# Performance work log

Hardware: AMD Instinct MI355X
Metric: run time of the kernel (lower is better)

## Reference

```python
import jax, jax.numpy as jnp
import numpy as np

NEG = -9e15

def _gat_layer(x, adj, W, a_src, a_dst):
    # x: [B,N,Fin], W: [Fin,Fout], a_src/a_dst: [Fout], adj: [N,N]
    h = jnp.einsum('bnf,fo->bno', x, W)                    # [B,N,Fout]
    e_src = jnp.einsum('bno,o->bn', h, a_src)              # [B,N]
    e_dst = jnp.einsum('bno,o->bn', h, a_dst)              # [B,N]
    e = jax.nn.leaky_relu(e_src[:, :, None] + e_dst[:, None, :], 0.2)  # [B,N,N]
    att = jax.nn.softmax(jnp.where(adj > 0, e, NEG), axis=-1)
    return jnp.einsum('bij,bjo->bio', att, h)              # [B,N,Fout]

def setup_inputs() -> dict:
    key = jax.random.key(0)
    ks = jax.random.split(key, 12)
    B, N, Fin = 8, 2048, 128
    H = [128, 128, 64]
    C = 128
    s = lambda *d: 1.0 / np.sqrt(d[0])
    inp = {
        'x':   jax.random.normal(ks[0], (B, N, Fin), jnp.float32),
        'adj': jax.random.normal(ks[1], (N, N), jnp.float32),
        'W1':  jax.random.normal(ks[2], (Fin, H[0]), jnp.float32) * s(Fin),
        'a1s': jax.random.normal(ks[3], (H[0],), jnp.float32) * s(H[0]),
        'a1d': jax.random.normal(ks[4], (H[0],), jnp.float32) * s(H[0]),
        'W2':  jax.random.normal(ks[5], (H[0], H[1]), jnp.float32) * s(H[0]),
        'a2s': jax.random.normal(ks[6], (H[1],), jnp.float32) * s(H[1]),
        'a2d': jax.random.normal(ks[7], (H[1],), jnp.float32) * s(H[1]),
        'W3':  jax.random.normal(ks[8], (H[1], H[2]), jnp.float32) * s(H[1]),
        'a3s': jax.random.normal(ks[9], (H[2],), jnp.float32) * s(H[2]),
        'a3d': jax.random.normal(ks[10], (H[2],), jnp.float32) * s(H[2]),
        'Wlin': jax.random.normal(ks[11], (H[2] * N, C), jnp.float32) * s(H[2] * N),
        'blin': jnp.zeros((C,), jnp.float32),
    }
    return inp

def reference(x, adj, W1, a1s, a1d, W2, a2s, a2d, W3, a3s, a3d, Wlin, blin):
    out = jax.nn.relu(_gat_layer(x, adj, W1, a1s, a1d))
    out = jax.nn.relu(_gat_layer(out, adj, W2, a2s, a2d))
    out = jax.nn.relu(_gat_layer(out, adj, W3, a3s, a3d))
    B = out.shape[0]
    out = out.reshape(B, -1)              # flatten [B, N*H3]
    return out @ Wlin + blin              # [B, num_classes]
```

## Files before the change

kernel.cpp:

```cpp
#include <hip/hip_runtime.h>
#include <stdint.h>


typedef unsigned short u16;
typedef __bf16 bf16x8 __attribute__((ext_vector_type(8)));
typedef float f32x4 __attribute__((ext_vector_type(4)));
typedef u16 u16x8 __attribute__((ext_vector_type(8)));

#define LOG2E 1.44269504088896340736f

__device__ __forceinline__ float b2f(u16 u) {
    union { unsigned int i; float f; } v; v.i = ((unsigned int)u) << 16; return v.f;
}
__device__ __forceinline__ u16 f2b(float f) {
    union { float f; unsigned int i; } v; v.f = f;
    unsigned int i = v.i;
    return (u16)((i + 0x7fffu + ((i >> 16) & 1u)) >> 16);
}
__device__ __forceinline__ float fast_exp2(float x) {
#if __has_builtin(__builtin_amdgcn_exp2f)
    return __builtin_amdgcn_exp2f(x);
#else
    return exp2f(x);
#endif
}

union ABfrag { bf16x8 v; u16x8 u; };

__device__ __forceinline__ void gload_lds16(const u16* g, u16* l) {
    __builtin_amdgcn_global_load_lds((const __attribute__((address_space(1))) void*)g,
                                     (__attribute__((address_space(3))) void*)l,
                                     16, 0, 0);
}

__global__ void __launch_bounds__(256) k_mask(const float* __restrict__ adj,
                                              uint32_t* __restrict__ adjm) {
    const int w = threadIdx.x >> 6, lane = threadIdx.x & 63;
    const int row = blockIdx.x * 4 + w;
    const float* ar = adj + (size_t)row * 2048;
    uint32_t* mr = adjm + (size_t)row * 64;
    for (int j0 = 0; j0 < 2048; j0 += 64) {
        unsigned long long m = __ballot(ar[j0 + lane] > 0.f);
        if (lane == 0) {
            mr[(j0 >> 5)] = (uint32_t)m;
            mr[(j0 >> 5) + 1] = (uint32_t)(m >> 32);
        }
    }
}

__global__ void k_prep(const float* __restrict__ W1, const float* __restrict__ W2,
                       const float* __restrict__ W3,
                       const float* __restrict__ a1s, const float* __restrict__ a1d,
                       const float* __restrict__ a2s, const float* __restrict__ a2d,
                       const float* __restrict__ a3s, const float* __restrict__ a3d,
                       u16* __restrict__ Wt1, u16* __restrict__ Wt2, u16* __restrict__ Wt3,
                       float* __restrict__ u1s, float* __restrict__ u1d,
                       float* __restrict__ u2s, float* __restrict__ u2d,
                       float* __restrict__ u3s, float* __restrict__ u3d) {
    if (blockIdx.x == 160) {
        int f = threadIdx.x;
        if (f < 128) {
            float s1 = 0.f, d1 = 0.f, s2 = 0.f, d2 = 0.f, s3 = 0.f, d3 = 0.f;
            for (int o = 0; o < 128; ++o) { float w = W1[f * 128 + o]; s1 += w * a1s[o]; d1 += w * a1d[o]; }
            for (int o = 0; o < 128; ++o) { float w = W2[f * 128 + o]; s2 += w * a2s[o]; d2 += w * a2d[o]; }
            for (int o = 0; o <  64; ++o) { float w = W3[f *  64 + o]; s3 += w * a3s[o]; d3 += w * a3d[o]; }
            u1s[f] = s1 * LOG2E; u1d[f] = d1 * LOG2E;
            u2s[f] = s2 * LOG2E; u2d[f] = d2 * LOG2E;
            u3s[f] = s3 * LOG2E; u3d[f] = d3 * LOG2E;
        }
        return;
    }
    int idx = blockIdx.x * 256 + threadIdx.x;
    if (idx < 16384) {
        int f = idx >> 7, o = idx & 127;
        Wt1[o * 128 + f] = f2b(W1[idx]);
    } else if (idx < 32768) {
        int j = idx - 16384; int f = j >> 7, o = j & 127;
        Wt2[o * 128 + f] = f2b(W2[j]);
    } else if (idx < 40960) {
        int j = idx - 32768; int f = j >> 6, o = j & 63;
        Wt3[o * 128 + f] = f2b(W3[j]);
    }
}

template <int F, bool XF32>
__global__ void __launch_bounds__(256) k_h(const void* __restrict__ xv,
                                           const u16* __restrict__ Wt,
                                           const float* __restrict__ us,
                                           const float* __restrict__ ud,
                                           u16* __restrict__ h_t,
                                           float* __restrict__ es2,
                                           float* __restrict__ ed2) {
    constexpr int NT = F / 16;
    constexpr int TNP = 72;
    __shared__ __align__(16) u16 hl[F * TNP];

    const int b = blockIdx.x;
    const int nblk = blockIdx.y;
    const int tid = threadIdx.x;
    const int w = tid >> 6, lane = tid & 63;
    const int quad = lane >> 4, l15 = lane & 15;
    const int n0w = nblk * 64 + w * 16;
    const int i_a = n0w + l15;

    ABfrag afr[4];
    float ps = 0.f, pd = 0.f;
    if (XF32) {
        const float* xr = (const float*)xv + ((size_t)(b * 2048 + i_a)) * 128;
#pragma unroll
        for (int kk = 0; kk < 4; ++kk) {
            const int o8 = kk * 32 + quad * 8;
            float4 x0 = *reinterpret_cast<const float4*>(xr + o8);
            float4 x1 = *reinterpret_cast<const float4*>(xr + o8 + 4);
            float4 s0 = *reinterpret_cast<const float4*>(us + o8);
            float4 s1 = *reinterpret_cast<const float4*>(us + o8 + 4);
            float4 d0 = *reinterpret_cast<const float4*>(ud + o8);
            float4 d1 = *reinterpret_cast<const float4*>(ud + o8 + 4);
            ps += x0.x * s0.x + x0.y * s0.y + x0.z * s0.z + x0.w * s0.w
                + x1.x * s1.x + x1.y * s1.y + x1.z * s1.z + x1.w * s1.w;
            pd += x0.x * d0.x + x0.y * d0.y + x0.z * d0.z + x0.w * d0.w
                + x1.x * d1.x + x1.y * d1.y + x1.z * d1.z + x1.w * d1.w;
            afr[kk].u[0] = f2b(x0.x); afr[kk].u[1] = f2b(x0.y);
            afr[kk].u[2] = f2b(x0.z); afr[kk].u[3] = f2b(x0.w);
            afr[kk].u[4] = f2b(x1.x); afr[kk].u[5] = f2b(x1.y);
            afr[kk].u[6] = f2b(x1.z); afr[kk].u[7] = f2b(x1.w);
        }
    } else {
        const u16* xr = (const u16*)xv + ((size_t)(b * 2048 + i_a)) * 128;
#pragma unroll
        for (int kk = 0; kk < 4; ++kk) {
            const int o8 = kk * 32 + quad * 8;
            u16x8 xa = *reinterpret_cast<const u16x8*>(xr + o8);
            afr[kk].u = xa;
            float4 s0 = *reinterpret_cast<const float4*>(us + o8);
            float4 s1 = *reinterpret_cast<const float4*>(us + o8 + 4);
            float4 d0 = *reinterpret_cast<const float4*>(ud + o8);
            float4 d1 = *reinterpret_cast<const float4*>(ud + o8 + 4);
            float xf[8];
#pragma unroll
            for (int j = 0; j < 8; ++j) xf[j] = b2f(xa[j]);
            ps += xf[0] * s0.x + xf[1] * s0.y + xf[2] * s0.z + xf[3] * s0.w
                + xf[4] * s1.x + xf[5] * s1.y + xf[6] * s1.z + xf[7] * s1.w;
            pd += xf[0] * d0.x + xf[1] * d0.y + xf[2] * d0.z + xf[3] * d0.w
                + xf[4] * d1.x + xf[5] * d1.y + xf[6] * d1.z + xf[7] * d1.w;
        }
    }
    ps += __shfl_xor(ps, 16, 64); ps += __shfl_xor(ps, 32, 64);
    pd += __shfl_xor(pd, 16, 64); pd += __shfl_xor(pd, 32, 64);
    if (quad == 0) {
        es2[b * 2048 + i_a] = ps;
        ed2[b * 2048 + i_a] = pd;
    }

    f32x4 acc[NT];
#pragma unroll
    for (int nt = 0; nt < NT; ++nt) acc[nt] = (f32x4){0.f, 0.f, 0.f, 0.f};
#pragma unroll
    for (int kk = 0; kk < 4; ++kk) {
#pragma unroll
        for (int nt = 0; nt < NT; ++nt) {
            bf16x8 bfv = *reinterpret_cast<const bf16x8*>(
                Wt + (nt * 16 + l15) * 128 + kk * 32 + quad * 8);
            acc[nt] = __builtin_amdgcn_mfma_f32_16x16x32_bf16(afr[kk].v, bfv, acc[nt], 0, 0, 0);
        }
    }

#pragma unroll
    for (int nt = 0; nt < NT; ++nt)
#pragma unroll
        for (int r = 0; r < 4; ++r)
            hl[(nt * 16 + l15) * TNP + w * 16 + quad * 4 + r] = f2b(acc[nt][r]);
    __syncthreads();
    if (tid < F * 2) {
        int o = tid >> 1, half = tid & 1;
        const u16* src = hl + o * TNP + half * 32;
        u16* dst = h_t + ((size_t)(b * F + o)) * 2048 + nblk * 64 + half * 32;
#pragma unroll
        for (int c = 0; c < 4; ++c)
            *reinterpret_cast<u16x8*>(dst + c * 8) =
                *reinterpret_cast<const u16x8*>(src + c * 8);
    }
}

template <int F, bool OUT_F32>
__global__ void __launch_bounds__(512) k_attn(const float* __restrict__ es2,
                                              const float* __restrict__ ed2,
                                              const uint32_t* __restrict__ adjm,
                                              const u16* __restrict__ h_t,
                                              void* __restrict__ outp) {
    constexpr int NT = F / 16;
    __shared__ __align__(16) u16 Ht[2][2][F * 64];
    __shared__ float dLDS[2][64];
    float* accLDS = (float*)&Ht[0][0][0];

    const int b = blockIdx.x;
    const int iblk = blockIdx.y;
    const int tid = threadIdx.x;
    const int grp = tid >> 8;
    const int t8 = tid & 255;
    const int w = t8 >> 6;
    const int lane = tid & 63;
    const int quad = lane >> 4, l15 = lane & 15;
    const int i_a = iblk * 64 + w * 16 + l15;

    const float esv = es2[b * 2048 + i_a];
    const float* edb = ed2 + b * 2048;
    const uint2* mrow = (const uint2*)(adjm + (size_t)i_a * 64);
    const u16* hb = h_t + (size_t)b * F * 2048;

    const int lro = lane >> 3;
    const int lcp = lane & 7;
    const int jt0 = grp * 16;

    f32x4 acc[NT];
#pragma unroll
    for (int nt = 0; nt < NT; ++nt) acc[nt] = (f32x4){0.f, 0.f, 0.f, 0.f};
    float dacc = 0.f;

    {
        const int j0 = jt0 * 64;
#pragma unroll
        for (int it = 0; it < F / 32; ++it) {
            int ro = (it * 4 + w) * 8 + lro;
            int c = lcp ^ (ro & 7);
            gload_lds16(hb + (size_t)ro * 2048 + j0 + c * 8, &Ht[grp][0][(it * 4 + w) * 512]);
        }
    }
    float4 ec0 = *reinterpret_cast<const float4*>(edb + jt0 * 64 + quad * 8);
    float4 ec1 = *reinterpret_cast<const float4*>(edb + jt0 * 64 + quad * 8 + 4);
    float4 ec2 = *reinterpret_cast<const float4*>(edb + jt0 * 64 + quad * 8 + 32);
    float4 ec3 = *reinterpret_cast<const float4*>(edb + jt0 * 64 + quad * 8 + 36);
    uint2 mc = mrow[jt0];
    __syncthreads();

    for (int jj = 0; jj < 16; ++jj) {
        const int cur = jj & 1, nxt = cur ^ 1;
        float4 en0, en1, en2, en3; uint2 mn;
        if (jj < 15) {
            const int j1 = (jt0 + jj + 1) * 64;
#pragma unroll
            for (int it = 0; it < F / 32; ++it) {
                int ro = (it * 4 + w) * 8 + lro;
                int c = lcp ^ (ro & 7);
                gload_lds16(hb + (size_t)ro * 2048 + j1 + c * 8, &Ht[grp][nxt][(it * 4 + w) * 512]);
            }
            en0 = *reinterpret_cast<const float4*>(edb + j1 + quad * 8);
            en1 = *reinterpret_cast<const float4*>(edb + j1 + quad * 8 + 4);
            en2 = *reinterpret_cast<const float4*>(edb + j1 + quad * 8 + 32);
            en3 = *reinterpret_cast<const float4*>(edb + j1 + quad * 8 + 36);
            mn = mrow[jt0 + jj + 1];
        }

        ABfrag af[2];
        {
            float ed[16] = {ec0.x, ec0.y, ec0.z, ec0.w, ec1.x, ec1.y, ec1.z, ec1.w,
                            ec2.x, ec2.y, ec2.z, ec2.w, ec3.x, ec3.y, ec3.z, ec3.w};
#pragma unroll
            for (int kk = 0; kk < 2; ++kk) {
                uint32_t word = kk ? mc.y : mc.x;
#pragma unroll
                for (int jx = 0; jx < 8; ++jx) {
                    float e = esv + ed[kk * 8 + jx];
                    float v = fmaxf(e, 0.2f * e);
                    float wv = fast_exp2(v);
                    bool bit = (word >> (quad * 8 + jx)) & 1u;
                    wv = bit ? wv : 0.f;
                    u16 wb = f2b(wv);
                    af[kk].u[jx] = wb;
                    dacc += b2f(wb);
                }
            }
        }

#pragma unroll
        for (int kk = 0; kk < 2; ++kk) {
#pragma unroll
            for (int nt = 0; nt < NT; ++nt) {
                int ob = nt * 16 + l15;
                int c = kk * 4 + quad;
                bf16x8 bfv = *reinterpret_cast<const bf16x8*>(
                    &Ht[grp][cur][ob * 64 + ((c ^ (ob & 7)) * 8)]);
                acc[nt] = __builtin_amdgcn_mfma_f32_16x16x32_bf16(af[kk].v, bfv, acc[nt], 0, 0, 0);
            }
        }

        if (jj < 15) { ec0 = en0; ec1 = en1; ec2 = en2; ec3 = en3; mc = mn; }
        __syncthreads();
    }

    dacc += __shfl_xor(dacc, 16, 64);
    dacc += __shfl_xor(dacc, 32, 64);
    if (quad == 0) dLDS[grp][w * 16 + l15] = dacc;
    if (grp == 1) {
#pragma unroll
        for (int nt = 0; nt < NT; ++nt)
            *reinterpret_cast<f32x4*>(&accLDS[(t8 * NT + nt) * 4]) = acc[nt];
    }
    __syncthreads();
    if (grp == 0) {
#pragma unroll
        for (int nt = 0; nt < NT; ++nt)
            acc[nt] += *reinterpret_cast<const f32x4*>(&accLDS[(t8 * NT + nt) * 4]);
        float dinv[4];
#pragma unroll
        for (int r = 0; r < 4; ++r) {
            int row = w * 16 + quad * 4 + r;
            dinv[r] = 1.0f / fmaxf(dLDS[0][row] + dLDS[1][row], 1e-30f);
        }
        const int ib = iblk * 64 + w * 16 + quad * 4;
        if (OUT_F32) {
            float* o3 = (float*)outp;
#pragma unroll
            for (int nt = 0; nt < NT; ++nt)
#pragma unroll
                for (int r = 0; r < 4; ++r) {
                    float vv = fmaxf(acc[nt][r] * dinv[r], 0.f);
                    o3[((size_t)(b * 2048 + ib + r)) * F + nt * 16 + l15] = vv;
                }
        } else {
            u16* xo = (u16*)outp;
#pragma unroll
            for (int nt = 0; nt < NT; ++nt)
#pragma unroll
                for (int r = 0; r < 4; ++r) {
                    float vv = fmaxf(acc[nt][r] * dinv[r], 0.f);
                    xo[((size_t)(b * 2048 + ib + r)) * F + nt * 16 + l15] = f2b(vv);
                }
        }
    }
}

__global__ void __launch_bounds__(256) k_lin(const float* __restrict__ o3,
                                             const float* __restrict__ Wlin,
                                             float* __restrict__ pbuf) {
    __shared__ float xc[8][256];
    __shared__ float red[8][8][128];
    const int tid = threadIdx.x;
    const int k0 = blockIdx.x * 256;
    for (int idx = tid; idx < 2048; idx += 256) {
        int bb = idx >> 8, kk = idx & 255;
        xc[bb][kk] = o3[(size_t)bb * 131072 + k0 + kk];
    }
    __syncthreads();
    const int o4 = tid & 31;
    const int kb = tid >> 5;
    f32x4 acc[8];
#pragma unroll
    for (int bb = 0; bb < 8; ++bb) acc[bb] = (f32x4){0.f, 0.f, 0.f, 0.f};
    const float* wp = Wlin + (size_t)(k0 + kb * 32) * 128 + o4 * 4;
#pragma unroll 4
    for (int k = 0; k < 32; ++k) {
        f32x4 wv = *reinterpret_cast<const f32x4*>(wp + (size_t)k * 128);
#pragma unroll
        for (int bb = 0; bb < 8; ++bb) acc[bb] += wv * xc[bb][kb * 32 + k];
    }
#pragma unroll
    for (int bb = 0; bb < 8; ++bb)
        *reinterpret_cast<f32x4*>(&red[kb][bb][o4 * 4]) = acc[bb];
    __syncthreads();
    const int f = tid * 4;
    const int bb = f >> 7, o = f & 127;
    f32x4 s = (f32x4){0.f, 0.f, 0.f, 0.f};
#pragma unroll
    for (int k2 = 0; k2 < 8; ++k2) s += *reinterpret_cast<const f32x4*>(&red[k2][bb][o]);
    *reinterpret_cast<f32x4*>(&pbuf[(size_t)blockIdx.x * 1024 + f]) = s;
}

__global__ void __launch_bounds__(256) k_bias(const float* __restrict__ pbuf,
                                              const float* __restrict__ blin,
                                              float* __restrict__ out) {
    __shared__ float red[256];
    const int tid = threadIdx.x;
    const int p16 = tid >> 4;
    const int fo = tid & 15;
    const int f0 = blockIdx.x * 16;
    float s = 0.f;
#pragma unroll 4
    for (int p = p16; p < 512; p += 16)
        s += pbuf[(size_t)p * 1024 + f0 + fo];
    red[tid] = s;
    __syncthreads();
    if (tid < 16) {
        float t = 0.f;
#pragma unroll
        for (int k = 0; k < 16; ++k) t += red[k * 16 + tid];
        out[f0 + tid] = t + blin[(f0 + tid) & 127];
    }
}

extern "C" void kernel_launch(void* const* d_in, const int* in_sizes, int n_in,
                              void* d_out, int out_size, void* d_ws, size_t ws_size,
                              hipStream_t stream) {
    (void)in_sizes; (void)n_in; (void)out_size;
    const float* x    = (const float*)d_in[0];
    const float* adj  = (const float*)d_in[1];
    const float* W1   = (const float*)d_in[2];
    const float* a1s  = (const float*)d_in[3];
    const float* a1d  = (const float*)d_in[4];
    const float* W2   = (const float*)d_in[5];
    const float* a2s  = (const float*)d_in[6];
    const float* a2d  = (const float*)d_in[7];
    const float* W3   = (const float*)d_in[8];
    const float* a3s  = (const float*)d_in[9];
    const float* a3d  = (const float*)d_in[10];
    const float* Wlin = (const float*)d_in[11];
    const float* blin = (const float*)d_in[12];

    char* ws = (char*)d_ws;
    u16*   h_t = (u16*)ws;
    size_t off = (size_t)4 << 20;
    float* es2 = (float*)(ws + off); off += 65536;
    float* ed2 = (float*)(ws + off); off += 65536;
    u16*   Wt1 = (u16*)(ws + off);   off += 32768;
    u16*   Wt2 = (u16*)(ws + off);   off += 32768;
    u16*   Wt3 = (u16*)(ws + off);   off += 16384;
    float* u1s = (float*)(ws + off); off += 512;
    float* u1d = (float*)(ws + off); off += 512;
    float* u2s = (float*)(ws + off); off += 512;
    float* u2d = (float*)(ws + off); off += 512;
    float* u3s = (float*)(ws + off); off += 512;
    float* u3d = (float*)(ws + off); off += 512;
    uint32_t* adjm = (uint32_t*)(ws + off); off += 524288;
    float* pbuf = (float*)(ws + off); off += (size_t)512 * 1024 * 4;
    u16* actA;
    if (ws_size >= off + ((size_t)4 << 20)) {
        actA = (u16*)(ws + off);
    } else {
        actA = (u16*)d_in[0];
    }
    float* o3 = (float*)actA;

    dim3 g(8, 32);
    k_mask<<<512, 256, 0, stream>>>(adj, adjm);
    k_prep<<<161, 256, 0, stream>>>(W1, W2, W3, a1s, a1d, a2s, a2d, a3s, a3d,
                                    Wt1, Wt2, Wt3, u1s, u1d, u2s, u2d, u3s, u3d);

    k_h<128, true ><<<g, 256, 0, stream>>>((const void*)x, Wt1, u1s, u1d, h_t, es2, ed2);
    k_attn<128, false><<<g, 512, 0, stream>>>(es2, ed2, adjm, h_t, (void*)actA);

    k_h<128, false><<<g, 256, 0, stream>>>((const void*)actA, Wt2, u2s, u2d, h_t, es2, ed2);
    k_attn<128, false><<<g, 512, 0, stream>>>(es2, ed2, adjm, h_t, (void*)actA);

    k_h<64, false><<<g, 256, 0, stream>>>((const void*)actA, Wt3, u3s, u3d, h_t, es2, ed2);
    k_attn<64, true ><<<g, 512, 0, stream>>>(es2, ed2, adjm, h_t, (void*)o3);

    k_lin<<<512, 256, 0, stream>>>(o3, Wlin, pbuf);
    k_bias<<<64, 256, 0, stream>>>(pbuf, blin, (float*)d_out);
}
```

Measured before the change: 259.8 us.

## Restructure attention kernel: register-loaded H fragments, split-K across waves, 32-row tiles

```diff
diff --git a/kernel.cpp b/kernel.cpp
--- a/kernel.cpp
+++ b/kernel.cpp
@@ -26,12 +26,6 @@
 }
 
 union ABfrag { bf16x8 v; u16x8 u; };
-
-__device__ __forceinline__ void gload_lds16(const u16* g, u16* l) {
-    __builtin_amdgcn_global_load_lds((const __attribute__((address_space(1))) void*)g,
-                                     (__attribute__((address_space(3))) void*)l,
-                                     16, 0, 0);
-}
 
 __global__ void __launch_bounds__(256) k_mask(const float* __restrict__ adj,
                                               uint32_t* __restrict__ adjm) {
@@ -183,149 +177,126 @@
 }
 
 template <int F, bool OUT_F32>
-__global__ void __launch_bounds__(512) k_attn(const float* __restrict__ es2,
-                                              const float* __restrict__ ed2,
-                                              const uint32_t* __restrict__ adjm,
-                                              const u16* __restrict__ h_t,
-                                              void* __restrict__ outp) {
+__global__ void __launch_bounds__(256, 2) k_attn(const float* __restrict__ es2,
+                                                 const float* __restrict__ ed2,
+                                                 const uint32_t* __restrict__ adjm,
+                                                 const u16* __restrict__ h_t,
+                                                 void* __restrict__ outp) {
     constexpr int NT = F / 16;
-    __shared__ __align__(16) u16 Ht[2][2][F * 64];
-    __shared__ float dLDS[2][64];
-    float* accLDS = (float*)&Ht[0][0][0];
+    __shared__ float accL[4][32][F];
+    __shared__ float dL[4][32];
 
     const int b = blockIdx.x;
     const int iblk = blockIdx.y;
     const int tid = threadIdx.x;
-    const int grp = tid >> 8;
-    const int t8 = tid & 255;
-    const int w = t8 >> 6;
-    const int lane = tid & 63;
+    const int w = tid >> 6, lane = tid & 63;
     const int quad = lane >> 4, l15 = lane & 15;
-    const int i_a = iblk * 64 + w * 16 + l15;
-
-    const float esv = es2[b * 2048 + i_a];
+    const int i0 = iblk * 32;
+
     const float* edb = ed2 + b * 2048;
-    const uint2* mrow = (const uint2*)(adjm + (size_t)i_a * 64);
-    const u16* hb = h_t + (size_t)b * F * 2048;
-
-    const int lro = lane >> 3;
-    const int lcp = lane & 7;
-    const int jt0 = grp * 16;
-
-    f32x4 acc[NT];
-#pragma unroll
-    for (int nt = 0; nt < NT; ++nt) acc[nt] = (f32x4){0.f, 0.f, 0.f, 0.f};
-    float dacc = 0.f;
-
-    {
-        const int j0 = jt0 * 64;
-#pragma unroll
-        for (int it = 0; it < F / 32; ++it) {
-            int ro = (it * 4 + w) * 8 + lro;
-            int c = lcp ^ (ro & 7);
-            gload_lds16(hb + (size_t)ro * 2048 + j0 + c * 8, &Ht[grp][0][(it * 4 + w) * 512]);
-        }
-    }
-    float4 ec0 = *reinterpret_cast<const float4*>(edb + jt0 * 64 + quad * 8);
-    float4 ec1 = *reinterpret_cast<const float4*>(edb + jt0 * 64 + quad * 8 + 4);
-    float4 ec2 = *reinterpret_cast<const float4*>(edb + jt0 * 64 + quad * 8 + 32);
-    float4 ec3 = *reinterpret_cast<const float4*>(edb + jt0 * 64 + quad * 8 + 36);
-    uint2 mc = mrow[jt0];
+    const u16* hb = h_t + (size_t)b * F * 2048 + (size_t)l15 * 2048;
+    float esv0 = es2[b * 2048 + i0 + l15];
+    float esv1 = es2[b * 2048 + i0 + 16 + l15];
+    const uint32_t* mr0 = adjm + (size_t)(i0 + l15) * 64 + w * 16;
+    const uint32_t* mr1 = adjm + (size_t)(i0 + 16 + l15) * 64 + w * 16;
+    const int j0w = w * 512 + quad * 8;
+
+    f32x4 acc[2][NT];
+#pragma unroll
+    for (int ig = 0; ig < 2; ++ig)
+#pragma unroll
+        for (int nt = 0; nt < NT; ++nt) acc[ig][nt] = (f32x4){0.f, 0.f, 0.f, 0.f};
+    float dacc0 = 0.f, dacc1 = 0.f;
+
+    ABfrag Br[2][NT];
+    float4 e0r[2], e1r[2];
+    uint32_t m0r[2], m1r[2];
+
+#pragma unroll
+    for (int nt = 0; nt < NT; ++nt)
+        Br[0][nt].u = *reinterpret_cast<const u16x8*>(hb + (size_t)nt * 16 * 2048 + j0w);
+    e0r[0] = *reinterpret_cast<const float4*>(edb + j0w);
+    e1r[0] = *reinterpret_cast<const float4*>(edb + j0w + 4);
+    m0r[0] = mr0[0]; m1r[0] = mr1[0];
+
+#pragma unroll
+    for (int s = 0; s < 16; ++s) {
+        const int cur = s & 1, nxt = cur ^ 1;
+        if (s < 15) {
+            const int jn = j0w + (s + 1) * 32;
+#pragma unroll
+            for (int nt = 0; nt < NT; ++nt)
+                Br[nxt][nt].u = *reinterpret_cast<const u16x8*>(hb + (size_t)nt * 16 * 2048 + jn);
+            e0r[nxt] = *reinterpret_cast<const float4*>(edb + jn);
+            e1r[nxt] = *reinterpret_cast<const float4*>(edb + jn + 4);
+            m0r[nxt] = mr0[s + 1]; m1r[nxt] = mr1[s + 1];
+        }
+        float ed[8] = {e0r[cur].x, e0r[cur].y, e0r[cur].z, e0r[cur].w,
+                       e1r[cur].x, e1r[cur].y, e1r[cur].z, e1r[cur].w};
+        ABfrag af0, af1;
+#pragma unroll
+        for (int jj = 0; jj < 8; ++jj) {
+            float e = esv0 + ed[jj];
+            float v = fmaxf(e, 0.2f * e);
+            float wv = fast_exp2(v);
+            wv = ((m0r[cur] >> (quad * 8 + jj)) & 1u) ? wv : 0.f;
+            u16 wb = f2b(wv); af0.u[jj] = wb; dacc0 += b2f(wb);
+            e = esv1 + ed[jj];
+            v = fmaxf(e, 0.2f * e);
+            wv = fast_exp2(v);
+            wv = ((m1r[cur] >> (quad * 8 + jj)) & 1u) ? wv : 0.f;
+            wb = f2b(wv); af1.u[jj] = wb; dacc1 += b2f(wb);
+        }
+#pragma unroll
+        for (int nt = 0; nt < NT; ++nt) {
+            acc[0][nt] = __builtin_amdgcn_mfma_f32_16x16x32_bf16(af0.v, Br[cur][nt].v, acc[0][nt], 0, 0, 0);
+            acc[1][nt] = __builtin_amdgcn_mfma_f32_16x16x32_bf16(af1.v, Br[cur][nt].v, acc[1][nt], 0, 0, 0);
+        }
+    }
+
+    dacc0 += __shfl_xor(dacc0, 16, 64); dacc0 += __shfl_xor(dacc0, 32, 64);
+    dacc1 += __shfl_xor(dacc1, 16, 64); dacc1 += __shfl_xor(dacc1, 32, 64);
+    if (quad == 0) { dL[w][l15] = dacc0; dL[w][16 + l15] = dacc1; }
+#pragma unroll
+    for (int ig = 0; ig < 2; ++ig)
+#pragma unroll
+        for (int nt = 0; nt < NT; ++nt)
+#pragma unroll
+            for (int r = 0; r < 4; ++r)
+                accL[w][ig * 16 + quad * 4 + r][nt * 16 + l15] = acc[ig][nt][r];
     __syncthreads();
 
-    for (int jj = 0; jj < 16; ++jj) {
-        const int cur = jj & 1, nxt = cur ^ 1;
-        float4 en0, en1, en2, en3; uint2 mn;
-        if (jj < 15) {
-            const int j1 = (jt0 + jj + 1) * 64;
-#pragma unroll
-            for (int it = 0; it < F / 32; ++it) {
-                int ro = (it * 4 + w) * 8 + lro;
-                int c = lcp ^ (ro & 7);
-                gload_lds16(hb + (size_t)ro * 2048 + j1 + c * 8, &Ht[grp][nxt][(it * 4 + w) * 512]);
+    const int i = tid >> 3;
+    constexpr int nf = F / 8;
+    const int f0 = (tid & 7) * nf;
+    const float den = dL[0][i] + dL[1][i] + dL[2][i] + dL[3][i];
+    const float dinv = 1.0f / fmaxf(den, 1e-30f);
+    const size_t rowoff = ((size_t)(b * 2048 + i0 + i)) * F + f0;
+    if (OUT_F32) {
+        float* o3 = (float*)outp;
+#pragma unroll
+        for (int k = 0; k < nf; k += 4) {
+            f32x4 s4 = *reinterpret_cast<const f32x4*>(&accL[0][i][f0 + k]);
+            s4 += *reinterpret_cast<const f32x4*>(&accL[1][i][f0 + k]);
+            s4 += *reinterpret_cast<const f32x4*>(&accL[2][i][f0 + k]);
+            s4 += *reinterpret_cast<const f32x4*>(&accL[3][i][f0 + k]);
+            f32x4 v;
+#pragma unroll
+            for (int c = 0; c < 4; ++c) v[c] = fmaxf(s4[c] * dinv, 0.f);
+            *reinterpret_cast<f32x4*>((float*)o3 + rowoff + k) = v;
+        }
+    } else {
+        u16* xo = (u16*)outp;
+#pragma unroll
+        for (int k = 0; k < nf; k += 8) {
+            u16x8 pk;
+#pragma unroll
+            for (int c = 0; c < 8; ++c) {
+                float sv = accL[0][i][f0 + k + c] + accL[1][i][f0 + k + c]
+                         + accL[2][i][f0 + k + c] + accL[3][i][f0 + k + c];
+                pk[c] = f2b(fmaxf(sv * dinv, 0.f));
             }
-            en0 = *reinterpret_cast<const float4*>(edb + j1 + quad * 8);
-            en1 = *reinterpret_cast<const float4*>(edb + j1 + quad * 8 + 4);
-            en2 = *reinterpret_cast<const float4*>(edb + j1 + quad * 8 + 32);
-            en3 = *reinterpret_cast<const float4*>(edb + j1 + quad * 8 + 36);
-            mn = mrow[jt0 + jj + 1];
-        }
-
-        ABfrag af[2];
-        {
-            float ed[16] = {ec0.x, ec0.y, ec0.z, ec0.w, ec1.x, ec1.y, ec1.z, ec1.w,
-                            ec2.x, ec2.y, ec2.z, ec2.w, ec3.x, ec3.y, ec3.z, ec3.w};
-#pragma unroll
-            for (int kk = 0; kk < 2; ++kk) {
-                uint32_t word = kk ? mc.y : mc.x;
-#pragma unroll
-                for (int jx = 0; jx < 8; ++jx) {
-                    float e = esv + ed[kk * 8 + jx];
-                    float v = fmaxf(e, 0.2f * e);
-                    float wv = fast_exp2(v);
-                    bool bit = (word >> (quad * 8 + jx)) & 1u;
-                    wv = bit ? wv : 0.f;
-                    u16 wb = f2b(wv);
-                    af[kk].u[jx] = wb;
-                    dacc += b2f(wb);
-                }
-            }
-        }
-
-#pragma unroll
-        for (int kk = 0; kk < 2; ++kk) {
-#pragma unroll
-            for (int nt = 0; nt < NT; ++nt) {
-                int ob = nt * 16 + l15;
-                int c = kk * 4 + quad;
-                bf16x8 bfv = *reinterpret_cast<const bf16x8*>(
-                    &Ht[grp][cur][ob * 64 + ((c ^ (ob & 7)) * 8)]);
-                acc[nt] = __builtin_amdgcn_mfma_f32_16x16x32_bf16(af[kk].v, bfv, acc[nt], 0, 0, 0);
-            }
-        }
-
-        if (jj < 15) { ec0 = en0; ec1 = en1; ec2 = en2; ec3 = en3; mc = mn; }
-        __syncthreads();
-    }
-
-    dacc += __shfl_xor(dacc, 16, 64);
-    dacc += __shfl_xor(dacc, 32, 64);
-    if (quad == 0) dLDS[grp][w * 16 + l15] = dacc;
-    if (grp == 1) {
-#pragma unroll
-        for (int nt = 0; nt < NT; ++nt)
-            *reinterpret_cast<f32x4*>(&accLDS[(t8 * NT + nt) * 4]) = acc[nt];
-    }
-    __syncthreads();
-    if (grp == 0) {
-#pragma unroll
-        for (int nt = 0; nt < NT; ++nt)
-            acc[nt] += *reinterpret_cast<const f32x4*>(&accLDS[(t8 * NT + nt) * 4]);
-        float dinv[4];
-#pragma unroll
-        for (int r = 0; r < 4; ++r) {
-            int row = w * 16 + quad * 4 + r;
-            dinv[r] = 1.0f / fmaxf(dLDS[0][row] + dLDS[1][row], 1e-30f);
-        }
-        const int ib = iblk * 64 + w * 16 + quad * 4;
-        if (OUT_F32) {
-            float* o3 = (float*)outp;
-#pragma unroll
-            for (int nt = 0; nt < NT; ++nt)
-#pragma unroll
-                for (int r = 0; r < 4; ++r) {
-                    float vv = fmaxf(acc[nt][r] * dinv[r], 0.f);
-                    o3[((size_t)(b * 2048 + ib + r)) * F + nt * 16 + l15] = vv;
-                }
-        } else {
-            u16* xo = (u16*)outp;
-#pragma unroll
-            for (int nt = 0; nt < NT; ++nt)
-#pragma unroll
-                for (int r = 0; r < 4; ++r) {
-                    float vv = fmaxf(acc[nt][r] * dinv[r], 0.f);
-                    xo[((size_t)(b * 2048 + ib + r)) * F + nt * 16 + l15] = f2b(vv);
-                }
+            *reinterpret_cast<u16x8*>(xo + rowoff + k) = pk;
         }
     }
 }
@@ -430,19 +401,20 @@
     }
     float* o3 = (float*)actA;
 
-    dim3 g(8, 32);
+    dim3 gh(8, 32);
+    dim3 ga(8, 64);
     k_mask<<<512, 256, 0, stream>>>(adj, adjm);
     k_prep<<<161, 256, 0, stream>>>(W1, W2, W3, a1s, a1d, a2s, a2d, a3s, a3d,
                                     Wt1, Wt2, Wt3, u1s, u1d, u2s, u2d, u3s, u3d);
 
-    k_h<128, true ><<<g, 256, 0, stream>>>((const void*)x, Wt1, u1s, u1d, h_t, es2, ed2);
-    k_attn<128, false><<<g, 512, 0, stream>>>(es2, ed2, adjm, h_t, (void*)actA);
-
-    k_h<128, false><<<g, 256, 0, stream>>>((const void*)actA, Wt2, u2s, u2d, h_t, es2, ed2);
-    k_attn<128, false><<<g, 512, 0, stream>>>(es2, ed2, adjm, h_t, (void*)actA);
-
-    k_h<64, false><<<g, 256, 0, stream>>>((const void*)actA, Wt3, u3s, u3d, h_t, es2, ed2);
-    k_attn<64, true ><<<g, 512, 0, stream>>>(es2, ed2, adjm, h_t, (void*)o3);
+    k_h<128, true ><<<gh, 256, 0, stream>>>((const void*)x, Wt1, u1s, u1d, h_t, es2, ed2);
+    k_attn<128, false><<<ga, 256, 0, stream>>>(es2, ed2, adjm, h_t, (void*)actA);
+
+    k_h<128, false><<<gh, 256, 0, stream>>>((const void*)actA, Wt2, u2s, u2d, h_t, es2, ed2);
+    k_attn<128, false><<<ga, 256, 0, stream>>>(es2, ed2, adjm, h_t, (void*)actA);
+
+    k_h<64, false><<<gh, 256, 0, stream>>>((const void*)actA, Wt3, u3s, u3d, h_t, es2, ed2);
+    k_attn<64, true ><<<ga, 256, 0, stream>>>(es2, ed2, adjm, h_t, (void*)o3);
 
     k_lin<<<512, 256, 0, stream>>>(o3, Wlin, pbuf);
     k_bias<<<64, 256, 0, stream>>>(pbuf, blin, (float*)d_out);
```

Measured after the change: 385.2 us. 48.3% more time.
